# Optimization experiments

Measured on AMD Instinct MI355X. Metric: run time of the kernel, lower is better.

## Reference

```python
import jax, jax.numpy as jnp
import numpy as np

N_EMB = 512
EMB_DIM = 64
DECAY = 0.99
EPS = 1e-5


def setup_inputs() -> dict:
    key = jax.random.key(0)
    k1, k2 = jax.random.split(key)
    x = jax.random.normal(k1, (32, EMB_DIM, 64, 64), dtype=jnp.float32)
    weight = jax.random.uniform(k2, (EMB_DIM, N_EMB), dtype=jnp.float32)  # rd_init=True: torch.rand(emb_dim, n_emb)
    cluster_size = jnp.zeros((N_EMB,), dtype=jnp.float32)
    embed_avg = weight  # buffer initialized as embed.clone()
    return {"x": x, "weight": weight, "cluster_size": cluster_size, "embed_avg": embed_avg}


def reference(x, weight, cluster_size, embed_avg):
    B, D, H, W = x.shape
    n_emb = weight.shape[1]
    # (B, D, H, W) -> (N, D) tokens
    flat = jnp.transpose(x, (0, 2, 3, 1)).reshape(-1, D)
    dist = (jnp.sum(flat * flat, axis=1, keepdims=True)
            - 2.0 * (flat @ weight)
            + jnp.sum(weight * weight, axis=0)[None, :])
    argmin = jnp.argmin(dist, axis=1)                      # (N,)
    quant = jnp.take(weight.T, argmin, axis=0)             # gather -> (N, D)
    result = jnp.transpose(quant.reshape(B, H, W, D), (0, 3, 1, 2))  # (B, D, H, W)

    # --- EMA codebook update (training branch) ---
    ones = jnp.ones(argmin.shape, dtype=x.dtype)
    n_idx = jax.ops.segment_sum(ones, argmin, num_segments=n_emb)    # onehot.sum(0)
    n_idx = jnp.where(n_idx == 0, jnp.ones_like(n_idx), n_idx)       # clamp empty clusters to 1
    new_cluster_size = DECAY * cluster_size + (1.0 - DECAY) * n_idx
    embed_sum = jax.ops.segment_sum(flat, argmin, num_segments=n_emb).T  # flatten.T @ onehot -> (D, n_emb)
    new_embed_avg = DECAY * embed_avg + (1.0 - DECAY) * embed_sum
    n = jnp.sum(new_cluster_size)
    cs = (new_cluster_size + EPS) / (n + n_emb * EPS) * n
    new_weight = new_embed_avg / cs[None, :]

    return result, argmin.reshape(B, H, W), new_weight, new_cluster_size, new_embed_avg
```

## Files before the change

### kernel.cpp

```cpp
#include <hip/hip_runtime.h>

#define NEMB 512
#define EMB 64
#define BSTR 262144
#define DECAYF 0.99f
#define OMDF 0.01f
#define EPSF 1e-5f
#define GAP_T 0.012f
#define QCAP 32768

typedef __attribute__((ext_vector_type(8))) short bf16x8;
typedef __attribute__((ext_vector_type(4))) float f32x4;

__device__ __forceinline__ unsigned short f2bf(float f) {
    unsigned u = __float_as_uint(f);
    return (unsigned short)((u + 0x7FFFu + ((u >> 16) & 1u)) >> 16);
}
__device__ __forceinline__ float bf2f(unsigned short h) {
    return __uint_as_float(((unsigned)h) << 16);
}

__global__ void prep_kernel(const float* __restrict__ w,
                            unsigned short* __restrict__ wh, unsigned short* __restrict__ wl,
                            float* __restrict__ wsq,
                            float* __restrict__ cnt_ws, float* __restrict__ es_region,
                            unsigned* __restrict__ gcnt) {
    int j = threadIdx.x;
    if (blockIdx.x < 8) {
        int d0 = blockIdx.x << 3;
        bf16x8 hb, lb;
#pragma unroll
        for (int i = 0; i < 8; ++i) {
            float v = w[(d0 + i) * NEMB + j];
            unsigned short h = f2bf(v);
            hb[i] = (short)h;
            lb[i] = (short)f2bf(v - bf2f(h));
        }
        *(bf16x8*)(wh + j * EMB + d0) = hb;
        *(bf16x8*)(wl + j * EMB + d0) = lb;
    } else {
        float s = 0.f;
#pragma unroll
        for (int d = 0; d < EMB; ++d) { float v = w[d * NEMB + j]; s = fmaf(v, v, s); }
        wsq[j] = s;
        cnt_ws[j] = 0.f;
        if (j == 0) *gcnt = 0u;
#pragma unroll
        for (int k = j; k < 32768; k += 512) es_region[k] = 0.f;
    }
}

#define UPD(S1, J1, S2, J2, s_, j_) do { \
    if (s_ < S1 || (s_ == S1 && j_ < J1)) { S2 = S1; J2 = J1; S1 = s_; J1 = j_; } \
    else if (s_ < S2 || (s_ == S2 && j_ < J2)) { S2 = s_; J2 = j_; } } while (0)

__global__ __launch_bounds__(512, 4) void vq_main(
    const float* __restrict__ x,
    const unsigned short* __restrict__ wh, const unsigned short* __restrict__ wl,
    const float* __restrict__ wsq,
    float* __restrict__ out_arg, unsigned* __restrict__ gcnt, int* __restrict__ queue)
{
    __shared__ __align__(16) unsigned char ubuf[65536];
    __shared__ float wsq_s[NEMB];
    __shared__ float xsq_s[256];

    float* xt = (float*)ubuf;
    unsigned short* whs = (unsigned short*)ubuf;
    unsigned short* wls = whs + 16384;

    const int tid = threadIdx.x;
    const int blk = blockIdx.x;
    const int b    = blk >> 4;
    const int hgrp = blk & 15;
    const int t0 = b * 4096 + hgrp * 256;
    const float* xbase = x + b * BSTR + hgrp * 256;

#pragma unroll
    for (int it = 0; it < 8; ++it) {
        int idx = tid + (it << 9);
        int d = idx >> 6, q = idx & 63;
        *(float4*)(xt + d * 256 + (q << 2)) = *(const float4*)(xbase + d * 4096 + (q << 2));
    }
    wsq_s[tid] = wsq[tid];
    __syncthreads();

    if (tid < 256) {
        float s = 0.f;
#pragma unroll
        for (int d = 0; d < EMB; ++d) { float v = xt[d * 256 + tid]; s = fmaf(v, v, s); }
        xsq_s[tid] = s;
    }

    const int lane = tid & 63;
    const int wave = tid >> 6;
    const int l15  = lane & 15;
    const int quad = lane >> 4;
    const int wbase = wave << 5;

    bf16x8 ah[2][2], al[2][2];
#pragma unroll
    for (int mt = 0; mt < 2; ++mt) {
        int m = wbase + (mt << 4) + l15;
#pragma unroll
        for (int ks = 0; ks < 2; ++ks) {
            int k0 = (ks << 5) + (quad << 3);
            bf16x8 hh, ll;
#pragma unroll
            for (int i = 0; i < 8; ++i) {
                float v = xt[(k0 + i) * 256 + m];
                unsigned short h = f2bf(v);
                hh[i] = (short)h;
                ll[i] = (short)f2bf(v - bf2f(h));
            }
            ah[mt][ks] = hh; al[mt][ks] = ll;
        }
    }
    __syncthreads();

    float xq[2][4];
#pragma unroll
    for (int mt = 0; mt < 2; ++mt)
#pragma unroll
        for (int r = 0; r < 4; ++r)
            xq[mt][r] = xsq_s[wbase + (mt << 4) + (quad << 2) + r];

    float v1[2][4], v2[2][4];
    int   j1[2][4];
#pragma unroll
    for (int mt = 0; mt < 2; ++mt)
#pragma unroll
        for (int r = 0; r < 4; ++r) { v1[mt][r] = 3.4e38f; v2[mt][r] = 3.4e38f; j1[mt][r] = 0; }

    const int m7 = l15 & 7;
    const int s0off = ((quad ^ m7) << 3);
    const int s1off = (((4 | quad) ^ m7) << 3);

    for (int half = 0; half < 2; ++half) {
#pragma unroll
        for (int it = 0; it < 8; ++it) {
            int e = tid + (it << 9);
            int arr  = e >> 11;
            int win  = e & 2047;
            int row  = win >> 3;
            int slot = win & 7;
            const unsigned short* src =
                (arr ? wl : wh) + ((half << 8) + row) * EMB + (slot << 3);
            bf16x8 v = *(const bf16x8*)src;
            unsigned short* dstb = arr ? wls : whs;
            *(bf16x8*)(dstb + row * EMB + ((slot ^ (row & 7)) << 3)) = v;
        }
        __syncthreads();

        const int nbase = half << 8;
#pragma unroll 2
        for (int it = 0; it < 16; ++it) {
            const int ib = ((it << 4) + l15) << 6;
            bf16x8 b0 = *(const bf16x8*)(whs + ib + s0off);
            bf16x8 b1 = *(const bf16x8*)(whs + ib + s1off);
            bf16x8 b2 = *(const bf16x8*)(wls + ib + s0off);
            bf16x8 b3 = *(const bf16x8*)(wls + ib + s1off);
            const int n = nbase + (it << 4) + l15;
            float wq = wsq_s[n];

            f32x4 acc0 = (f32x4){0.f, 0.f, 0.f, 0.f};
            f32x4 acc1 = (f32x4){0.f, 0.f, 0.f, 0.f};
            acc0 = __builtin_amdgcn_mfma_f32_16x16x32_bf16(ah[0][0], b0, acc0, 0, 0, 0);
            acc1 = __builtin_amdgcn_mfma_f32_16x16x32_bf16(ah[1][0], b0, acc1, 0, 0, 0);
            acc0 = __builtin_amdgcn_mfma_f32_16x16x32_bf16(ah[0][1], b1, acc0, 0, 0, 0);
            acc1 = __builtin_amdgcn_mfma_f32_16x16x32_bf16(ah[1][1], b1, acc1, 0, 0, 0);
            acc0 = __builtin_amdgcn_mfma_f32_16x16x32_bf16(ah[0][0], b2, acc0, 0, 0, 0);
            acc1 = __builtin_amdgcn_mfma_f32_16x16x32_bf16(ah[1][0], b2, acc1, 0, 0, 0);
            acc0 = __builtin_amdgcn_mfma_f32_16x16x32_bf16(ah[0][1], b3, acc0, 0, 0, 0);
            acc1 = __builtin_amdgcn_mfma_f32_16x16x32_bf16(ah[1][1], b3, acc1, 0, 0, 0);
            acc0 = __builtin_amdgcn_mfma_f32_16x16x32_bf16(al[0][0], b0, acc0, 0, 0, 0);
            acc1 = __builtin_amdgcn_mfma_f32_16x16x32_bf16(al[1][0], b0, acc1, 0, 0, 0);
            acc0 = __builtin_amdgcn_mfma_f32_16x16x32_bf16(al[0][1], b1, acc0, 0, 0, 0);
            acc1 = __builtin_amdgcn_mfma_f32_16x16x32_bf16(al[1][1], b1, acc1, 0, 0, 0);

#pragma unroll
            for (int r = 0; r < 4; ++r) {
                float s0 = fmaf(-2.f, acc0[r], xq[0][r] + wq);
                bool p0 = s0 < v1[0][r];
                float mx0 = fmaxf(s0, v1[0][r]);
                v1[0][r] = fminf(s0, v1[0][r]);
                v2[0][r] = fminf(v2[0][r], mx0);
                j1[0][r] = p0 ? n : j1[0][r];

                float s1 = fmaf(-2.f, acc1[r], xq[1][r] + wq);
                bool p1 = s1 < v1[1][r];
                float mx1 = fmaxf(s1, v1[1][r]);
                v1[1][r] = fminf(s1, v1[1][r]);
                v2[1][r] = fminf(v2[1][r], mx1);
                j1[1][r] = p1 ? n : j1[1][r];
            }
        }
        __syncthreads();
    }

#pragma unroll
    for (int mt = 0; mt < 2; ++mt)
#pragma unroll
        for (int r = 0; r < 4; ++r) {
            float a1 = v1[mt][r], a2 = v2[mt][r];
            int   aj = j1[mt][r];
#pragma unroll
            for (int msk = 1; msk < 16; msk <<= 1) {
                float o1 = __shfl_xor(a1, msk, 64);
                int   oj = __shfl_xor(aj, msk, 64);
                float o2 = __shfl_xor(a2, msk, 64);
                bool take = (o1 < a1) || (o1 == a1 && oj < aj);
                float mx = fmaxf(a1, o1);
                a2 = fminf(fminf(a2, o2), mx);
                a1 = fminf(a1, o1);
                aj = take ? oj : aj;
            }
            v1[mt][r] = a1; v2[mt][r] = a2; j1[mt][r] = aj;
        }

    if (l15 == 0) {
#pragma unroll
        for (int mt = 0; mt < 2; ++mt)
#pragma unroll
            for (int r = 0; r < 4; ++r) {
                int gt = t0 + wbase + (mt << 4) + (quad << 2) + r;
                out_arg[gt] = (float)j1[mt][r];
                if (v2[mt][r] - v1[mt][r] < GAP_T) {
                    unsigned idx = atomicAdd(gcnt, 1u);
                    if (idx < QCAP) queue[idx] = gt;
                }
            }
    }
}

__global__ __launch_bounds__(256) void refine_kernel(
    const float* __restrict__ x, const float* __restrict__ w,
    const float* __restrict__ wsq, const unsigned* __restrict__ gcnt,
    const int* __restrict__ queue, float* __restrict__ out_arg)
{
    __shared__ float wsq_s[NEMB];
    const int tid = threadIdx.x;
    wsq_s[tid] = wsq[tid];
    wsq_s[tid + 256] = wsq[tid + 256];
    __syncthreads();

    unsigned nfu = *gcnt;
    const int nf = (int)(nfu < (unsigned)QCAP ? nfu : (unsigned)QCAP);
    const int lane = tid & 63;
    const int gw = (blockIdx.x << 2) + (tid >> 6);

    for (int i = gw; i < nf; i += 1024) {
        const int t = queue[i];
        const int b = t >> 12, pos = t & 4095;
        float xd = x[b * BSTR + lane * 4096 + pos];
        float xqv = xd * xd;
#pragma unroll
        for (int mk = 1; mk < 64; mk <<= 1) xqv += __shfl_xor(xqv, mk, 64);

        float accv[8];
#pragma unroll
        for (int k = 0; k < 8; ++k) accv[k] = 0.f;
#pragma unroll 4
        for (int d = 0; d < EMB; ++d) {
            float4 wa = *(const float4*)(w + d * NEMB + (lane << 2));
            float4 wb = *(const float4*)(w + d * NEMB + 256 + (lane << 2));
            float xv = __shfl(xd, d, 64);
            accv[0] = fmaf(xv, wa.x, accv[0]);
            accv[1] = fmaf(xv, wa.y, accv[1]);
            accv[2] = fmaf(xv, wa.z, accv[2]);
            accv[3] = fmaf(xv, wa.w, accv[3]);
            accv[4] = fmaf(xv, wb.x, accv[4]);
            accv[5] = fmaf(xv, wb.y, accv[5]);
            accv[6] = fmaf(xv, wb.z, accv[6]);
            accv[7] = fmaf(xv, wb.w, accv[7]);
        }

        float S1 = 3.4e38f, S2 = 3.4e38f; int J1 = 0, J2 = 0;
#pragma unroll
        for (int k = 0; k < 8; ++k) {
            int j = (k < 4) ? ((lane << 2) + k) : (256 + (lane << 2) + k - 4);
            float s = (xqv - 2.f * accv[k]) + wsq_s[j];
            UPD(S1, J1, S2, J2, s, j);
        }
#pragma unroll
        for (int mk = 1; mk < 64; mk <<= 1) {
            float os1 = __shfl_xor(S1, mk, 64); int oj1 = __shfl_xor(J1, mk, 64);
            float os2 = __shfl_xor(S2, mk, 64); int oj2 = __shfl_xor(J2, mk, 64);
            UPD(S1, J1, S2, J2, os1, oj1);
            UPD(S1, J1, S2, J2, os2, oj2);
        }

        int jm = J1;
        if (S2 - S1 < 1e-3f) {
            float w1 = w[lane * NEMB + J1];
            float w2 = w[lane * NEMB + J2];
            double e1 = (double)w1 * (double)w1 - 2.0 * (double)xd * (double)w1;
            double e2 = (double)w2 * (double)w2 - 2.0 * (double)xd * (double)w2;
#pragma unroll
            for (int mk = 1; mk < 64; mk <<= 1) {
                e1 += __shfl_xor(e1, mk, 64);
                e2 += __shfl_xor(e2, mk, 64);
            }
            if (e2 < e1 || (e2 == e1 && J2 < J1)) jm = J2;
        }
        if (lane == 0) out_arg[t] = (float)jm;
    }
}

__global__ __launch_bounds__(512) void finish_kernel(
    const float* __restrict__ x, const float* __restrict__ w, const float* __restrict__ arg,
    float* __restrict__ out_result,
    float* __restrict__ es, float* __restrict__ cnt)
{
    __shared__ float wrow8[8 * 512];
    __shared__ float acc8[8 * 513];
    __shared__ float cacc[513];
    const int tid = threadIdx.x;
    const int grp = blockIdx.x >> 6;
    const int chunk = blockIdx.x & 63;

#pragma unroll
    for (int d = 0; d < 8; ++d) {
        wrow8[(d << 9) + tid] = w[((grp << 3) + d) * NEMB + tid];
        acc8[d * 513 + tid] = 0.f;
    }
    if (tid < 8) acc8[tid * 513 + 512] = 0.f;
    cacc[tid] = 0.f;
    if (tid == 0) cacc[512] = 0.f;
    __syncthreads();

    const int t = (chunk << 11) + (tid << 2);
    const int b = t >> 12;
    const int o = b * BSTR + (t & 4095);
    float4 a4 = *(const float4*)(arg + t);
    int j0 = (int)a4.x, j1 = (int)a4.y, j2 = (int)a4.z, j3 = (int)a4.w;
    if (grp == 0) {
        atomicAdd(&cacc[j0], 1.f);
        atomicAdd(&cacc[j1], 1.f);
        atomicAdd(&cacc[j2], 1.f);
        atomicAdd(&cacc[j3], 1.f);
    }
#pragma unroll
    for (int d = 0; d < 8; ++d) {
        const int dg = (grp << 3) + d;
        float4 x4 = *(const float4*)(x + o + dg * 4096);
        float* ad = acc8 + d * 513;
        atomicAdd(&ad[j0], x4.x);
        atomicAdd(&ad[j1], x4.y);
        atomicAdd(&ad[j2], x4.z);
        atomicAdd(&ad[j3], x4.w);
        float4 r4 = {wrow8[(d << 9) + j0], wrow8[(d << 9) + j1],
                     wrow8[(d << 9) + j2], wrow8[(d << 9) + j3]};
        *(float4*)(out_result + o + dg * 4096) = r4;
    }
    __syncthreads();

#pragma unroll
    for (int d = 0; d < 8; ++d) {
        float v = acc8[d * 513 + tid];
        if (v != 0.f) atomicAdd(&es[((grp << 3) + d) * NEMB + tid], v);
    }
    if (grp == 0) {
        float cv = cacc[tid];
        if (cv != 0.f) atomicAdd(&cnt[tid], cv);
    }
}

__global__ void finalize_kernel(const float* __restrict__ cs_in, const float* __restrict__ avg_in,
                                const float* __restrict__ cnt_ws,
                                float* __restrict__ out_w, float* __restrict__ out_ncs,
                                float* __restrict__ avg_io ) {
    __shared__ float red[NEMB];
    const int j = threadIdx.x;
    const int d = blockIdx.x;
    float c = cnt_ws[j];
    float nidx = (c == 0.f) ? 1.f : c;
    float ncs = DECAYF * cs_in[j] + OMDF * nidx;
    red[j] = ncs;
    __syncthreads();
    for (int s = 256; s > 0; s >>= 1) {
        if (j < s) red[j] += red[j + s];
        __syncthreads();
    }
    float n = red[0];
    float csj = (ncs + EPSF) / (n + (float)NEMB * EPSF) * n;
    int o = d * NEMB + j;
    float esv = avg_io[o];
    float navg = DECAYF * avg_in[o] + OMDF * esv;
    avg_io[o] = navg;
    out_w[o] = navg / csj;
    if (d == 0) out_ncs[j] = ncs;
}

extern "C" void kernel_launch(void* const* d_in, const int* in_sizes, int n_in,
                              void* d_out, int out_size, void* d_ws, size_t ws_size,
                              hipStream_t stream) {
    (void)in_sizes; (void)n_in; (void)out_size; (void)ws_size;
    const float* x   = (const float*)d_in[0];
    const float* w   = (const float*)d_in[1];
    const float* cs  = (const float*)d_in[2];
    const float* avg = (const float*)d_in[3];

    float* out = (float*)d_out;
    float* out_result = out;
    float* out_arg    = out + 8388608;
    float* out_w      = out + 8519680;
    float* out_ncs    = out + 8552448;
    float* out_avg    = out + 8552960;

    char* wsb = (char*)d_ws;
    unsigned short* wh = (unsigned short*)wsb;
    unsigned short* wl = (unsigned short*)(wsb + 65536);
    float* wsq      = (float*)(wsb + 131072);
    float* cnt_ws   = (float*)(wsb + 133120);
    unsigned* gcnt  = (unsigned*)(wsb + 135168);
    int* queue      = (int*)(wsb + 135232);

    prep_kernel<<<9, 512, 0, stream>>>(w, wh, wl, wsq, cnt_ws, out_avg, gcnt);
    vq_main<<<512, 512, 0, stream>>>(x, wh, wl, wsq, out_arg, gcnt, queue);
    refine_kernel<<<256, 256, 0, stream>>>(x, w, wsq, gcnt, queue, out_arg);
    finish_kernel<<<512, 512, 0, stream>>>(x, w, out_arg, out_result, out_avg, cnt_ws);
    finalize_kernel<<<64, 512, 0, stream>>>(cs, avg, cnt_ws, out_w, out_ncs, out_avg);
}
```

Measured before the change: 189.7 us.

## Compute embed_sum via one-hot MFMA matmul with partial buffers instead of atomics

Replaces the atomic-based scatter for embed_sum with a dense one-hot matrix multiply on MFMA units, using x split into bf16 high and low parts. Each block writes its partial sums into a scratch area inside the result output buffer, and finalize reduces the 128 partials per entry. The result gather is moved into its own kernel that runs last, so it overwrites that scratch. This removes heavy LDS and global atomic contention, at the cost of extra MFMA work, an extra 16MB partial write and read, and a second read of x.

```diff
diff --git a/kernel.cpp b/kernel.cpp
--- a/kernel.cpp
+++ b/kernel.cpp
@@ -23,8 +23,7 @@
 __global__ void prep_kernel(const float* __restrict__ w,
                             unsigned short* __restrict__ wh, unsigned short* __restrict__ wl,
                             float* __restrict__ wsq,
-                            float* __restrict__ cnt_ws, float* __restrict__ es_region,
-                            unsigned* __restrict__ gcnt) {
+                            float* __restrict__ cnt_ws, unsigned* __restrict__ gcnt) {
     int j = threadIdx.x;
     if (blockIdx.x < 8) {
         int d0 = blockIdx.x << 3;
@@ -45,8 +44,6 @@
         wsq[j] = s;
         cnt_ws[j] = 0.f;
         if (j == 0) *gcnt = 0u;
-#pragma unroll
-        for (int k = j; k < 32768; k += 512) es_region[k] = 0.f;
     }
 }
 
@@ -249,7 +246,7 @@
     const int gw = (blockIdx.x << 2) + (tid >> 6);
 
     for (int i = gw; i < nf; i += 1024) {
-        const int t = queue[i];
+        const int t = queue[i] & 131071;
         const int b = t >> 12, pos = t & 4095;
         float xd = x[b * BSTR + lane * 4096 + pos];
         float xqv = xd * xd;
@@ -306,89 +303,166 @@
     }
 }
 
-__global__ __launch_bounds__(512) void finish_kernel(
-    const float* __restrict__ x, const float* __restrict__ w, const float* __restrict__ arg,
-    float* __restrict__ out_result,
-    float* __restrict__ es, float* __restrict__ cnt)
+__global__ __launch_bounds__(512) void es_kernel(
+    const float* __restrict__ x, const float* __restrict__ arg,
+    float* __restrict__ es_p, float* __restrict__ cnt_ws)
+{
+    __shared__ unsigned short xh[16384];
+    __shared__ unsigned short xl[16384];
+    __shared__ int args_s[256];
+    __shared__ float cacc[NEMB];
+
+    const int tid = threadIdx.x;
+    const int blk = blockIdx.x;
+    const int flavor = blk >> 7;
+    const int chunk = blk & 127;
+    const int b = chunk >> 2;
+    const int tpos0 = (chunk & 3) << 10;
+
+    cacc[tid] = 0.f;
+
+    const int lane = tid & 63;
+    const int wave = tid >> 6;
+    const int l15  = lane & 15;
+    const int quad = lane >> 4;
+    const int jb   = wave << 5;
+
+    f32x4 acc[4][2];
+#pragma unroll
+    for (int m = 0; m < 4; ++m)
+#pragma unroll
+        for (int nc = 0; nc < 2; ++nc) acc[m][nc] = (f32x4){0.f, 0.f, 0.f, 0.f};
+
+    for (int st = 0; st < 4; ++st) {
+        const int tpos = tpos0 + (st << 8);
+#pragma unroll
+        for (int it = 0; it < 8; ++it) {
+            int idx = tid + (it << 9);
+            int d = idx >> 6, q = idx & 63;
+            float4 g = *(const float4*)(x + b * BSTR + d * 4096 + tpos + (q << 2));
+            unsigned short h0 = f2bf(g.x), h1 = f2bf(g.y), h2 = f2bf(g.z), h3 = f2bf(g.w);
+            unsigned short e0 = f2bf(g.x - bf2f(h0)), e1 = f2bf(g.y - bf2f(h1));
+            unsigned short e2 = f2bf(g.z - bf2f(h2)), e3 = f2bf(g.w - bf2f(h3));
+            int c = q >> 1, half = q & 1;
+            int off = d * 256 + ((c ^ (d & 7)) << 3) + (half << 2);
+            ushort4 hv = {h0, h1, h2, h3};
+            ushort4 lv = {e0, e1, e2, e3};
+            *(ushort4*)(xh + off) = hv;
+            *(ushort4*)(xl + off) = lv;
+        }
+        if (tid < 256) args_s[tid] = ((int)arg[b * 4096 + tpos + tid]) & 511;
+        __syncthreads();
+
+        if (flavor == 0 && tid < 256) atomicAdd(&cacc[args_s[tid]], 1.f);
+
+#pragma unroll
+        for (int kk = 0; kk < 8; ++kk) {
+            bf16x8 ah[4], al[4];
+#pragma unroll
+            for (int m = 0; m < 4; ++m) {
+                int d = (m << 4) + l15;
+                int coff = ((((kk << 2) + quad) ^ (d & 7)) << 3);
+                ah[m] = *(const bf16x8*)(xh + d * 256 + coff);
+                al[m] = *(const bf16x8*)(xl + d * 256 + coff);
+            }
+            int argv[8];
+            const int kb = (kk << 5) + (quad << 3);
+#pragma unroll
+            for (int i = 0; i < 8; ++i) argv[i] = args_s[kb + i];
+#pragma unroll
+            for (int nc = 0; nc < 2; ++nc) {
+                const int jg = (flavor << 8) + jb + (nc << 4) + l15;
+                bf16x8 bf;
+#pragma unroll
+                for (int i = 0; i < 8; ++i) bf[i] = (argv[i] == jg) ? (short)0x3F80 : (short)0;
+#pragma unroll
+                for (int m = 0; m < 4; ++m) {
+                    acc[m][nc] = __builtin_amdgcn_mfma_f32_16x16x32_bf16(ah[m], bf, acc[m][nc], 0, 0, 0);
+                    acc[m][nc] = __builtin_amdgcn_mfma_f32_16x16x32_bf16(al[m], bf, acc[m][nc], 0, 0, 0);
+                }
+            }
+        }
+        __syncthreads();
+    }
+
+    float* ep = es_p + blk * 16384;
+#pragma unroll
+    for (int m = 0; m < 4; ++m)
+#pragma unroll
+        for (int nc = 0; nc < 2; ++nc) {
+            const int jl = jb + (nc << 4) + l15;
+#pragma unroll
+            for (int r = 0; r < 4; ++r) {
+                const int d = (m << 4) + (quad << 2) + r;
+                ep[d * 256 + jl] = acc[m][nc][r];
+            }
+        }
+    if (flavor == 0) {
+        float v = cacc[tid];
+        if (v != 0.f) atomicAdd(&cnt_ws[tid], v);
+    }
+}
+
+__global__ __launch_bounds__(256) void finalize_kernel(
+    const float* __restrict__ cs_in, const float* __restrict__ avg_in,
+    const float* __restrict__ cnt_ws, const float* __restrict__ es_p,
+    float* __restrict__ out_w, float* __restrict__ out_ncs,
+    float* __restrict__ out_avg) {
+    __shared__ float red[256];
+    const int tid = threadIdx.x;
+    const int d  = blockIdx.x >> 1;
+    const int jh = blockIdx.x & 1;
+
+    float c0 = cnt_ws[tid], c1 = cnt_ws[tid + 256];
+    float ncs0 = DECAYF * cs_in[tid] + OMDF * ((c0 == 0.f) ? 1.f : c0);
+    float ncs1 = DECAYF * cs_in[tid + 256] + OMDF * ((c1 == 0.f) ? 1.f : c1);
+    red[tid] = ncs0 + ncs1;
+    __syncthreads();
+    for (int s = 128; s > 0; s >>= 1) {
+        if (tid < s) red[tid] += red[tid + s];
+        __syncthreads();
+    }
+    const float n = red[0];
+
+    const float* ep = es_p + (jh << 7) * 16384 + d * 256 + tid;
+    float s = 0.f;
+#pragma unroll 16
+    for (int c = 0; c < 128; ++c) s += ep[c * 16384];
+
+    const float ncs = jh ? ncs1 : ncs0;
+    const float csj = (ncs + EPSF) / (n + (float)NEMB * EPSF) * n;
+    const int o = d * NEMB + (jh << 8) + tid;
+    const float navg = DECAYF * avg_in[o] + OMDF * s;
+    out_avg[o] = navg;
+    out_w[o] = navg / csj;
+    if (blockIdx.x == 0) { out_ncs[tid] = ncs0; out_ncs[tid + 256] = ncs1; }
+}
+
+__global__ __launch_bounds__(512) void result_kernel(
+    const float* __restrict__ w, const float* __restrict__ arg,
+    float* __restrict__ out_result)
 {
     __shared__ float wrow8[8 * 512];
-    __shared__ float acc8[8 * 513];
-    __shared__ float cacc[513];
     const int tid = threadIdx.x;
     const int grp = blockIdx.x >> 6;
     const int chunk = blockIdx.x & 63;
-
-#pragma unroll
-    for (int d = 0; d < 8; ++d) {
+#pragma unroll
+    for (int d = 0; d < 8; ++d)
         wrow8[(d << 9) + tid] = w[((grp << 3) + d) * NEMB + tid];
-        acc8[d * 513 + tid] = 0.f;
-    }
-    if (tid < 8) acc8[tid * 513 + 512] = 0.f;
-    cacc[tid] = 0.f;
-    if (tid == 0) cacc[512] = 0.f;
     __syncthreads();
 
     const int t = (chunk << 11) + (tid << 2);
-    const int b = t >> 12;
-    const int o = b * BSTR + (t & 4095);
+    const int o = (t >> 12) * BSTR + (t & 4095);
     float4 a4 = *(const float4*)(arg + t);
-    int j0 = (int)a4.x, j1 = (int)a4.y, j2 = (int)a4.z, j3 = (int)a4.w;
-    if (grp == 0) {
-        atomicAdd(&cacc[j0], 1.f);
-        atomicAdd(&cacc[j1], 1.f);
-        atomicAdd(&cacc[j2], 1.f);
-        atomicAdd(&cacc[j3], 1.f);
-    }
+    int j0 = ((int)a4.x) & 511, j1 = ((int)a4.y) & 511;
+    int j2 = ((int)a4.z) & 511, j3 = ((int)a4.w) & 511;
 #pragma unroll
     for (int d = 0; d < 8; ++d) {
         const int dg = (grp << 3) + d;
-        float4 x4 = *(const float4*)(x + o + dg * 4096);
-        float* ad = acc8 + d * 513;
-        atomicAdd(&ad[j0], x4.x);
-        atomicAdd(&ad[j1], x4.y);
-        atomicAdd(&ad[j2], x4.z);
-        atomicAdd(&ad[j3], x4.w);
         float4 r4 = {wrow8[(d << 9) + j0], wrow8[(d << 9) + j1],
                      wrow8[(d << 9) + j2], wrow8[(d << 9) + j3]};
         *(float4*)(out_result + o + dg * 4096) = r4;
     }
-    __syncthreads();
-
-#pragma unroll
-    for (int d = 0; d < 8; ++d) {
-        float v = acc8[d * 513 + tid];
-        if (v != 0.f) atomicAdd(&es[((grp << 3) + d) * NEMB + tid], v);
-    }
-    if (grp == 0) {
-        float cv = cacc[tid];
-        if (cv != 0.f) atomicAdd(&cnt[tid], cv);
-    }
-}
-
-__global__ void finalize_kernel(const float* __restrict__ cs_in, const float* __restrict__ avg_in,
-                                const float* __restrict__ cnt_ws,
-                                float* __restrict__ out_w, float* __restrict__ out_ncs,
-                                float* __restrict__ avg_io ) {
-    __shared__ float red[NEMB];
-    const int j = threadIdx.x;
-    const int d = blockIdx.x;
-    float c = cnt_ws[j];
-    float nidx = (c == 0.f) ? 1.f : c;
-    float ncs = DECAYF * cs_in[j] + OMDF * nidx;
-    red[j] = ncs;
-    __syncthreads();
-    for (int s = 256; s > 0; s >>= 1) {
-        if (j < s) red[j] += red[j + s];
-        __syncthreads();
-    }
-    float n = red[0];
-    float csj = (ncs + EPSF) / (n + (float)NEMB * EPSF) * n;
-    int o = d * NEMB + j;
-    float esv = avg_io[o];
-    float navg = DECAYF * avg_in[o] + OMDF * esv;
-    avg_io[o] = navg;
-    out_w[o] = navg / csj;
-    if (d == 0) out_ncs[j] = ncs;
 }
 
 extern "C" void kernel_launch(void* const* d_in, const int* in_sizes, int n_in,
@@ -406,6 +480,7 @@
     float* out_w      = out + 8519680;
     float* out_ncs    = out + 8552448;
     float* out_avg    = out + 8552960;
+    float* es_p       = out;
 
     char* wsb = (char*)d_ws;
     unsigned short* wh = (unsigned short*)wsb;
@@ -415,9 +490,10 @@
     unsigned* gcnt  = (unsigned*)(wsb + 135168);
     int* queue      = (int*)(wsb + 135232);
 
-    prep_kernel<<<9, 512, 0, stream>>>(w, wh, wl, wsq, cnt_ws, out_avg, gcnt);
+    prep_kernel<<<9, 512, 0, stream>>>(w, wh, wl, wsq, cnt_ws, gcnt);
     vq_main<<<512, 512, 0, stream>>>(x, wh, wl, wsq, out_arg, gcnt, queue);
     refine_kernel<<<256, 256, 0, stream>>>(x, w, wsq, gcnt, queue, out_arg);
-    finish_kernel<<<512, 512, 0, stream>>>(x, w, out_arg, out_result, out_avg, cnt_ws);
-    finalize_kernel<<<64, 512, 0, stream>>>(cs, avg, cnt_ws, out_w, out_ncs, out_avg);
-}
+    es_kernel<<<256, 512, 0, stream>>>(x, out_arg, es_p, cnt_ws);
+    finalize_kernel<<<128, 256, 0, stream>>>(cs, avg, cnt_ws, es_p, out_w, out_ncs, out_avg);
+    result_kernel<<<512, 512, 0, stream>>>(w, out_arg, out_result);
+}
```

Result: faster. 182.5 us (-3.8%).
